# Optimization experiments

Measured on AMD Instinct MI355X. Metric: run time of the kernel, lower is better.

## Reference

```python
import jax, jax.numpy as jnp
import numpy as np

SPATIAL_DECAY = 50.0
POS_SCALE = 1000.0  # spread positions so decay=50 gives realistic locality


def setup_inputs() -> dict:
    key = jax.random.key(0)
    k1, k2 = jax.random.split(key)
    N, D = 8192, 512
    features = jax.random.normal(k1, (N, D), dtype=jnp.float32)
    positions = jax.random.uniform(k2, (N, 2), dtype=jnp.float32) * POS_SCALE
    lambda_weight = jnp.asarray(0.5, dtype=jnp.float32)  # nn.Parameter init
    temperature = jnp.asarray(1.0, dtype=jnp.float32)    # nn.Parameter init
    return {"features": features, "positions": positions,
            "lambda_weight": lambda_weight, "temperature": temperature, "k": 20}


def reference(features, positions, lambda_weight, temperature, k):
    N = features.shape[0]
    # F.normalize(dim=1), eps=1e-12
    norms = jnp.linalg.norm(features, axis=1, keepdims=True)
    feat_norm = features / jnp.maximum(norms, 1e-12)
    sim = feat_norm @ feat_norm.T                                   # (N, N)
    # squared euclidean distances (cdist(p=2) then **2 == squared dist)
    sq = jnp.sum(positions * positions, axis=1)                      # (N,)
    d2 = jnp.maximum(sq[:, None] + sq[None, :] - 2.0 * (positions @ positions.T), 0.0)
    spatial = jnp.exp(-d2 / (2.0 * SPATIAL_DECAY ** 2))             # (N, N)
    lam = jax.nn.sigmoid(lambda_weight)
    adj = jax.nn.sigmoid((lam * sim + (1.0 - lam) * spatial) * temperature)
    # row-wise top-k mask, scatter 1.0 at top-k columns
    _, topk_idx = jax.lax.top_k(adj, k)                              # (N, k)
    rows = jnp.arange(N)[:, None]
    mask = jnp.zeros_like(adj).at[rows, topk_idx].set(1.0)
    return adj * mask, lam
```

## Files before the change

### kernel.cpp

```cpp
#include <hip/hip_runtime.h>
#include <hip/hip_fp16.h>
#include <math.h>

#define N 8192
#define D 512
#define KSEL 20
#define CAND_CAP 384
#define WINDOW 2.5e-3f
#define BS_EXTRA 6.2e-4f
#define ROWU 8192

typedef __attribute__((ext_vector_type(8))) short short8;
typedef __attribute__((ext_vector_type(4))) float f32x4;

__device__ __forceinline__ unsigned short f2bf(float x) {
  unsigned int u = __float_as_uint(x);
  unsigned int r = u + 0x7FFFu + ((u >> 16) & 1u);
  return (unsigned short)(r >> 16);
}

__device__ __forceinline__ unsigned int packh2(float a, float b) {
  return (unsigned int)__half_as_ushort(__float2half(a)) |
         ((unsigned int)__half_as_ushort(__float2half(b)) << 16);
}

__device__ __forceinline__ void gld16(const unsigned short* g, unsigned short* l) {
  __builtin_amdgcn_global_load_lds(
      (const __attribute__((address_space(1))) unsigned int*)g,
      (__attribute__((address_space(3))) unsigned int*)l, 16, 0, 0);
}

__global__ __launch_bounds__(256) void prep_kernel(
    const float* __restrict__ feat, const float* __restrict__ pos,
    const float* __restrict__ lamw,
    float* __restrict__ normf, float* __restrict__ sqf,
    float* __restrict__ out) {
  int row = blockIdx.x * 256 + threadIdx.x;
  if (row >= N) return;
  const float* f = feat + (size_t)row * D;
  float part[4];
  #pragma unroll
  for (int b = 0; b < 4; b++) {
    const float* a = f + b * 128;
    float r[8];
    #pragma unroll
    for (int j = 0; j < 8; j++) r[j] = __fmul_rn(a[j], a[j]);
    for (int i = 8; i < 128; i += 8) {
      #pragma unroll
      for (int j = 0; j < 8; j++)
        r[j] = __fadd_rn(r[j], __fmul_rn(a[i + j], a[i + j]));
    }
    part[b] = __fadd_rn(__fadd_rn(__fadd_rn(r[0], r[1]), __fadd_rn(r[2], r[3])),
                        __fadd_rn(__fadd_rn(r[4], r[5]), __fadd_rn(r[6], r[7])));
  }
  float s = __fadd_rn(__fadd_rn(part[0], part[1]), __fadd_rn(part[2], part[3]));
  float nrm = fmaxf(__fsqrt_rn(s), 1e-12f);
  normf[row] = nrm;
  float x = pos[2 * row], y = pos[2 * row + 1];
  sqf[row] = __fadd_rn(__fmul_rn(x, x), __fmul_rn(y, y));
  if (row == 0) {
    float e = (float)exp(-(double)lamw[0]);
    out[(size_t)N * N] = 1.0f / __fadd_rn(1.0f, e);
  }
}

__global__ __launch_bounds__(256) void fnorm_kernel(
    const float* __restrict__ feat, const float* __restrict__ normf,
    float* __restrict__ fn32, unsigned short* __restrict__ fnbf) {
  int i0 = (blockIdx.x * 256 + threadIdx.x) * 4;
  float n = normf[i0 >> 9];
  float4 v = *(const float4*)(feat + i0);
  float4 q;
  q.x = v.x / n; q.y = v.y / n; q.z = v.z / n; q.w = v.w / n;
  *(float4*)(fn32 + i0) = q;
  uint2 o;
  o.x = (unsigned int)f2bf(q.x) | ((unsigned int)f2bf(q.y) << 16);
  o.y = (unsigned int)f2bf(q.z) | ((unsigned int)f2bf(q.w) << 16);
  *(uint2*)(fnbf + i0) = o;
}

__global__ __launch_bounds__(256) void adj_kernel(
    const unsigned short* __restrict__ G,
    const float* __restrict__ pos, const float* __restrict__ sqf,
    const float* __restrict__ lamw, const float* __restrict__ temp,
    unsigned int* out_u) {
  __shared__ __align__(16) unsigned char smem[32768];
  unsigned short* As = (unsigned short*)smem;
  unsigned short* Bs = As + 8192;
  unsigned int* tileT = (unsigned int*)smem;

  int L = blockIdx.x;
  int tid = threadIdx.x;

  if (L < 2048) {
    uint4 z = {0u, 0u, 0u, 0u};
    #pragma unroll
    for (int it = 0; it < 16; it++) {
      int g = L * 16384 + it * 1024 + tid * 4;
      int r = g >> 12, c = g & 4095;
      *(uint4*)(out_u + (size_t)r * ROWU + 4096 + c) = z;
    }
  }

  int by = (int)((129.0 - sqrt(129.0 * 129.0 - 8.0 * (double)L)) * 0.5);
  while (64 * (by + 1) - ((by + 1) * by) / 2 <= L) by++;
  while (64 * by - (by * (by - 1)) / 2 > L) by--;
  int bx = by + (L - (64 * by - (by * (by - 1)) / 2));

  int wave = tid >> 6, lane = tid & 63;
  int wr = (wave >> 1) * 64, wc = (wave & 1) * 64;
  int m = lane & 15, quad = lane >> 4;

  f32x4 acc[4][4];
  #pragma unroll
  for (int i = 0; i < 4; i++)
    #pragma unroll
    for (int j = 0; j < 4; j++) acc[i][j] = (f32x4){0.f, 0.f, 0.f, 0.f};

  for (int kt = 0; kt < D / 64; kt++) {
    #pragma unroll
    for (int i = 0; i < 4; i++) {
      int f = i * 256 + tid;
      int r = f >> 3, c = f & 7;
      int cs = (c + r) & 7;
      size_t goff = (size_t)r * D + kt * 64 + cs * 8;
      gld16(G + (size_t)(by * 128) * D + goff, &As[f * 8]);
      gld16(G + (size_t)(bx * 128) * D + goff, &Bs[f * 8]);
    }
    __syncthreads();
    #pragma unroll
    for (int h = 0; h < 2; h++) {
      short8 fa[4], fb[4];
      #pragma unroll
      for (int ti = 0; ti < 4; ti++) {
        int row = wr + ti * 16 + m;
        int cc = ((h * 4 + quad) - row) & 7;
        fa[ti] = *(const short8*)&As[row * 64 + cc * 8];
      }
      #pragma unroll
      for (int tj = 0; tj < 4; tj++) {
        int row = wc + tj * 16 + m;
        int cc = ((h * 4 + quad) - row) & 7;
        fb[tj] = *(const short8*)&Bs[row * 64 + cc * 8];
      }
      #pragma unroll
      for (int ti = 0; ti < 4; ti++)
        #pragma unroll
        for (int tj = 0; tj < 4; tj++)
          acc[ti][tj] = __builtin_amdgcn_mfma_f32_16x16x32_bf16(
              fa[ti], fb[tj], acc[ti][tj], 0, 0, 0);
    }
    __syncthreads();
  }

  float lam = 1.f / (1.f + __expf(-lamw[0]));
  float T = temp[0];
  float oml = 1.f - lam;
  bool offdiag = (bx != by);
  #pragma unroll
  for (int ti = 0; ti < 4; ti++) {
    int gi0 = by * 128 + wr + ti * 16 + quad * 4;
    float xi[4], yi[4], sqi[4];
    #pragma unroll
    for (int r = 0; r < 4; r++) {
      int gi = gi0 + r;
      xi[r] = pos[2 * gi]; yi[r] = pos[2 * gi + 1]; sqi[r] = sqf[gi];
    }
    #pragma unroll
    for (int tj = 0; tj < 4; tj++) {
      int gj = bx * 128 + wc + tj * 16 + m;
      float xj = pos[2 * gj], yj = pos[2 * gj + 1], sj = sqf[gj];
      f32x4 c = acc[ti][tj];
      float sv[4];
      #pragma unroll
      for (int r = 0; r < 4; r++) {
        float d2 = fmaxf(sqi[r] + sj - 2.f * (xi[r] * xj + yi[r] * yj), 0.f);
        float sp = __expf(-d2 * (1.f / 5000.f));
        sv[r] = (lam * c[r] + oml * sp) * T;
      }
      #pragma unroll
      for (int r = 0; r < 4; r++) {
        float pv = __shfl_xor(sv[r], 1, 64);
        if (!(lane & 1))
          out_u[(size_t)(gi0 + r) * ROWU + (gj >> 1)] = packh2(sv[r], pv);
      }
      if (offdiag) {
        int colL = wc + tj * 16 + m;
        int p0 = (wr + ti * 16) / 2 + quad * 2;
        tileT[colL * 64 + (p0 ^ (colL & 31))]       = packh2(sv[0], sv[1]);
        tileT[colL * 64 + ((p0 + 1) ^ (colL & 31))] = packh2(sv[2], sv[3]);
      }
    }
  }
  if (offdiag) {
    __syncthreads();
    int p = tid & 63, c0 = tid >> 6;
    for (int it = 0; it < 32; it++) {
      int c = it * 4 + c0;
      unsigned int w = tileT[c * 64 + (p ^ (c & 31))];
      out_u[(size_t)(bx * 128 + c) * ROWU + (by * 64 + p)] = w;
    }
  }
}

__global__ __launch_bounds__(256, 6) void topk_kernel(
    const float* __restrict__ pos, const float* __restrict__ sqf,
    const float* __restrict__ lamw, const float* __restrict__ temp,
    const float* __restrict__ fn32, float* __restrict__ out) {
  __shared__ float Tm[64 * 64];
  __shared__ float ai[D];
  __shared__ int   redi[2][4];
  __shared__ int   candIdx[CAND_CAP];
  __shared__ float candV[CAND_CAP];
  __shared__ int   selIdx[KSEL];
  __shared__ float selVal[KSEL];
  __shared__ int   cnt;

  int row = blockIdx.x, t = threadIdx.x;
  int lane = t & 63, wid = t >> 6;
  float* orow = out + (size_t)row * N;
  const uint4* ou4 = (const uint4*)orow;
  const float* fn_i = fn32 + (size_t)row * D;

  float rv[32];
  #pragma unroll
  for (int q = 0; q < 4; q++) {
    uint4 u = ou4[t + 256 * q];
    unsigned int w[4] = {u.x, u.y, u.z, u.w};
    #pragma unroll
    for (int d = 0; d < 4; d++) {
      __half2 h2 = *reinterpret_cast<__half2*>(&w[d]);
      rv[8 * q + 2 * d]     = __low2float(h2);
      rv[8 * q + 2 * d + 1] = __high2float(h2);
    }
  }
  for (int k = t; k < D; k += 256) ai[k] = fn_i[k];
  if (t == 0) cnt = 0;
  __syncthreads();

  {
    float4 z4 = {0.f, 0.f, 0.f, 0.f};
    #pragma unroll
    for (int i = 0; i < 4; i++) *(float4*)&orow[4 * t + 1024 * i] = z4;
  }

  float lo = -1.0f, hi = 1.5f;
  for (int it = 0; it < 12; it++) {
    float mid = 0.5f * (lo + hi);
    int c = 0;
    #pragma unroll
    for (int q = 0; q < 32; q++) c += (rv[q] >= mid) ? 1 : 0;
    #pragma unroll
    for (int off = 32; off > 0; off >>= 1) c += __shfl_down(c, off, 64);
    if (lane == 0) redi[it & 1][wid] = c;
    __syncthreads();
    int tot = redi[it & 1][0] + redi[it & 1][1] + redi[it & 1][2] + redi[it & 1][3];
    if (tot >= KSEL) lo = mid; else hi = mid;
  }

  float thr = lo - (WINDOW + BS_EXTRA);
  #pragma unroll
  for (int q = 0; q < 32; q++) {
    if (rv[q] >= thr) {
      int p = atomicAdd(&cnt, 1);
      if (p < CAND_CAP) candIdx[p] = 8 * (t + 256 * (q >> 3)) + (q & 7);
    }
  }
  __syncthreads();
  int ncand = min(cnt, CAND_CAP);

  float lamf;
  { float e = (float)exp(-(double)lamw[0]); lamf = 1.0f / __fadd_rn(1.0f, e); }
  float omlf = __fadd_rn(1.0f, -lamf);
  float Tf = temp[0];
  float sq_i = sqf[row];
  float xi = pos[2 * row], yi = pos[2 * row + 1];
  int c4 = t >> 2, sub = t & 3;
  int slot = (c4 + 16 * sub) & 63;

  for (int g = 0; g < ncand; g += 64) {
    int sidx = g + c4;
    int sj = candIdx[(sidx < ncand) ? sidx : 0];
    const float* fj = fn32 + (size_t)sj * D + sub * 16;
    float accv = 0.0f;
    int myIdx = g + t;
    float4 pv[4];
    #pragma unroll
    for (int q = 0; q < 4; q++) pv[q] = *(const float4*)(fj + 0 * 64 + q * 4);
    for (int ck = 0; ck < 8; ck++) {
      __syncthreads();
      #pragma unroll
      for (int q = 0; q < 4; q++) {
        int kl = sub * 16 + q * 4;
        Tm[(kl + 0) * 64 + slot] = pv[q].x;
        Tm[(kl + 1) * 64 + slot] = pv[q].y;
        Tm[(kl + 2) * 64 + slot] = pv[q].z;
        Tm[(kl + 3) * 64 + slot] = pv[q].w;
      }
      __syncthreads();
      if (ck < 7) {
        #pragma unroll
        for (int q = 0; q < 4; q++) pv[q] = *(const float4*)(fj + (ck + 1) * 64 + q * 4);
      }
      if (t < 64) {
        int kk = ck * 64;
        for (int kl = 0; kl < 64; kl++) {
          int s = (t + 16 * (kl >> 4)) & 63;
          accv = __fmaf_rn(ai[kk + kl], Tm[kl * 64 + s], accv);
        }
      }
    }
    if (t < 64 && myIdx < ncand) {
      int j = candIdx[myIdx];
      float xj = pos[2 * j], yj = pos[2 * j + 1];
      float dot2 = __fmaf_rn(yi, yj, __fmul_rn(xi, xj));
      float Ssum = __fadd_rn(sq_i, sqf[j]);
      float d2 = fmaxf(__fadd_rn(Ssum, -__fmul_rn(2.0f, dot2)), 0.0f);
      float arg = (-d2) / 5000.0f;
      float sp = (float)exp((double)arg);
      float u = __fmul_rn(__fadd_rn(__fmul_rn(lamf, accv), __fmul_rn(omlf, sp)), Tf);
      float e = (float)exp(-(double)u);
      candV[myIdx] = 1.0f / __fadd_rn(1.0f, e);
    }
  }

  if (t < 64) {
    for (int s = 0; s < KSEL; s++) {
      float bu = -1.0f; int bj = N, bs = 0;
      for (int c = t; c < ncand; c += 64) {
        float v = candV[c]; int j = candIdx[c];
        if (v > bu || (v == bu && j < bj)) { bu = v; bj = j; bs = c; }
      }
      #pragma unroll
      for (int off = 32; off > 0; off >>= 1) {
        float ov = __shfl_down(bu, off, 64);
        int   oj = __shfl_down(bj, off, 64);
        int   os = __shfl_down(bs, off, 64);
        if (ov > bu || (ov == bu && oj < bj)) { bu = ov; bj = oj; bs = os; }
      }
      if (t == 0) { selIdx[s] = bj; selVal[s] = bu; candV[bs] = -1.0f; }
      __builtin_amdgcn_s_waitcnt(0);
    }
  }
  __syncthreads();
  if (t < KSEL) orow[selIdx[t]] = selVal[t];
}

extern "C" void kernel_launch(void* const* d_in, const int* in_sizes, int n_in,
                              void* d_out, int out_size, void* d_ws, size_t ws_size,
                              hipStream_t stream) {
  const float* feat = (const float*)d_in[0];
  const float* pos  = (const float*)d_in[1];
  const float* lamw = (const float*)d_in[2];
  const float* temp = (const float*)d_in[3];
  float* out = (float*)d_out;
  unsigned int* out_u = (unsigned int*)d_out;
  float* normf = (float*)d_ws;
  float* sqf   = normf + N;
  float* fn32  = sqf + N;
  unsigned short* fnbf = (unsigned short*)(fn32 + (size_t)N * D);

  prep_kernel<<<N / 256, 256, 0, stream>>>(feat, pos, lamw, normf, sqf, out);
  fnorm_kernel<<<(N * D) / 1024, 256, 0, stream>>>(feat, normf, fn32, fnbf);
  adj_kernel<<<2080, 256, 0, stream>>>(fnbf, pos, sqf, lamw, temp, out_u);
  topk_kernel<<<N, 256, 0, stream>>>(pos, sqf, lamw, temp, fn32, out);
}
```

Baseline: 588.1 us.

## Stage fp16 adjacency in workspace buffer, zero output in adj kernel, fuse prep

Merges the norm and normalize kernels into one warp-per-row prep kernel. When the workspace is large enough, the adjacency kernel writes the fp16 scores to a separate compact buffer through a swizzled LDS tile with 16-byte stores, and the transposed half is stored with vectorized writes too. The output is zeroed in contiguous chunks inside the adjacency kernel, so top-k no longer has to zero its row after reading it. The cost is extra workspace memory plus a fallback path that keeps the old in-place layout.

```diff
diff --git a/kernel.cpp b/kernel.cpp
--- a/kernel.cpp
+++ b/kernel.cpp
@@ -9,6 +9,7 @@
 #define WINDOW 2.5e-3f
 #define BS_EXTRA 6.2e-4f
 #define ROWU 8192
+#define FS_A 4096
 
 typedef __attribute__((ext_vector_type(8))) short short8;
 typedef __attribute__((ext_vector_type(4))) float f32x4;
@@ -30,60 +31,77 @@
       (__attribute__((address_space(3))) unsigned int*)l, 16, 0, 0);
 }
 
+__device__ __forceinline__ int swz(int row, int cp) {
+  return row * 64 + ((((cp >> 2) ^ (row & 15)) << 2) | (cp & 3));
+}
+__device__ __forceinline__ int swz4(int row, int q) {
+  return row * 64 + ((q ^ (row & 15)) << 2);
+}
+
 __global__ __launch_bounds__(256) void prep_kernel(
     const float* __restrict__ feat, const float* __restrict__ pos,
     const float* __restrict__ lamw,
     float* __restrict__ normf, float* __restrict__ sqf,
+    float* __restrict__ fn32, unsigned short* __restrict__ fnbf,
     float* __restrict__ out) {
-  int row = blockIdx.x * 256 + threadIdx.x;
-  if (row >= N) return;
-  const float* f = feat + (size_t)row * D;
-  float part[4];
-  #pragma unroll
-  for (int b = 0; b < 4; b++) {
-    const float* a = f + b * 128;
-    float r[8];
-    #pragma unroll
-    for (int j = 0; j < 8; j++) r[j] = __fmul_rn(a[j], a[j]);
-    for (int i = 8; i < 128; i += 8) {
-      #pragma unroll
-      for (int j = 0; j < 8; j++)
-        r[j] = __fadd_rn(r[j], __fmul_rn(a[i + j], a[i + j]));
-    }
-    part[b] = __fadd_rn(__fadd_rn(__fadd_rn(r[0], r[1]), __fadd_rn(r[2], r[3])),
-                        __fadd_rn(__fadd_rn(r[4], r[5]), __fadd_rn(r[6], r[7])));
-  }
-  float s = __fadd_rn(__fadd_rn(part[0], part[1]), __fadd_rn(part[2], part[3]));
-  float nrm = fmaxf(__fsqrt_rn(s), 1e-12f);
-  normf[row] = nrm;
-  float x = pos[2 * row], y = pos[2 * row + 1];
-  sqf[row] = __fadd_rn(__fmul_rn(x, x), __fmul_rn(y, y));
-  if (row == 0) {
-    float e = (float)exp(-(double)lamw[0]);
-    out[(size_t)N * N] = 1.0f / __fadd_rn(1.0f, e);
-  }
-}
-
-__global__ __launch_bounds__(256) void fnorm_kernel(
-    const float* __restrict__ feat, const float* __restrict__ normf,
-    float* __restrict__ fn32, unsigned short* __restrict__ fnbf) {
-  int i0 = (blockIdx.x * 256 + threadIdx.x) * 4;
-  float n = normf[i0 >> 9];
-  float4 v = *(const float4*)(feat + i0);
-  float4 q;
-  q.x = v.x / n; q.y = v.y / n; q.z = v.z / n; q.w = v.w / n;
-  *(float4*)(fn32 + i0) = q;
-  uint2 o;
-  o.x = (unsigned int)f2bf(q.x) | ((unsigned int)f2bf(q.y) << 16);
-  o.y = (unsigned int)f2bf(q.z) | ((unsigned int)f2bf(q.w) << 16);
-  *(uint2*)(fnbf + i0) = o;
+  __shared__ float rowbuf[4][512];
+  int w = threadIdx.x >> 6, lane = threadIdx.x & 63;
+  float* rb = rowbuf[w];
+  for (int i = 0; i < 8; i++) {
+    int row = blockIdx.x * 32 + w * 8 + i;
+    const float* f = feat + (size_t)row * D;
+    float4 v0 = *(const float4*)(f + 4 * lane);
+    float4 v1 = *(const float4*)(f + 256 + 4 * lane);
+    *(float4*)&rb[4 * lane] = v0;
+    *(float4*)&rb[256 + 4 * lane] = v1;
+    __builtin_amdgcn_s_waitcnt(0);
+    float s = 0.f;
+    if (lane < 32) {
+      int b = lane >> 3, j = lane & 7;
+      const float* a = rb + b * 128 + j;
+      float r = __fmul_rn(a[0], a[0]);
+      #pragma unroll
+      for (int k = 1; k < 16; k++)
+        r = __fadd_rn(r, __fmul_rn(a[8 * k], a[8 * k]));
+      r = __fadd_rn(r, __shfl_xor(r, 1, 64));
+      r = __fadd_rn(r, __shfl_xor(r, 2, 64));
+      r = __fadd_rn(r, __shfl_xor(r, 4, 64));
+      r = __fadd_rn(r, __shfl_xor(r, 8, 64));
+      r = __fadd_rn(r, __shfl_xor(r, 16, 64));
+      s = r;
+    }
+    float st = __shfl(s, 0, 64);
+    float nrm = fmaxf(__fsqrt_rn(st), 1e-12f);
+    if (lane == 0) {
+      normf[row] = nrm;
+      float x = pos[2 * row], y = pos[2 * row + 1];
+      sqf[row] = __fadd_rn(__fmul_rn(x, x), __fmul_rn(y, y));
+      if (row == 0) {
+        float e = (float)exp(-(double)lamw[0]);
+        out[(size_t)N * N] = 1.0f / __fadd_rn(1.0f, e);
+      }
+    }
+    float4 q0, q1;
+    q0.x = v0.x / nrm; q0.y = v0.y / nrm; q0.z = v0.z / nrm; q0.w = v0.w / nrm;
+    q1.x = v1.x / nrm; q1.y = v1.y / nrm; q1.z = v1.z / nrm; q1.w = v1.w / nrm;
+    *(float4*)(fn32 + (size_t)row * D + 4 * lane) = q0;
+    *(float4*)(fn32 + (size_t)row * D + 256 + 4 * lane) = q1;
+    uint2 o0, o1;
+    o0.x = (unsigned int)f2bf(q0.x) | ((unsigned int)f2bf(q0.y) << 16);
+    o0.y = (unsigned int)f2bf(q0.z) | ((unsigned int)f2bf(q0.w) << 16);
+    o1.x = (unsigned int)f2bf(q1.x) | ((unsigned int)f2bf(q1.y) << 16);
+    o1.y = (unsigned int)f2bf(q1.z) | ((unsigned int)f2bf(q1.w) << 16);
+    *(uint2*)(fnbf + (size_t)row * D + 4 * lane) = o0;
+    *(uint2*)(fnbf + (size_t)row * D + 256 + 4 * lane) = o1;
+  }
 }
 
 __global__ __launch_bounds__(256) void adj_kernel(
     const unsigned short* __restrict__ G,
     const float* __restrict__ pos, const float* __restrict__ sqf,
     const float* __restrict__ lamw, const float* __restrict__ temp,
-    unsigned int* out_u) {
+    unsigned int* __restrict__ filt, int fs,
+    unsigned int* __restrict__ out_u, int mode) {
   __shared__ __align__(16) unsigned char smem[32768];
   unsigned short* As = (unsigned short*)smem;
   unsigned short* Bs = As + 8192;
@@ -94,11 +112,18 @@
 
   if (L < 2048) {
     uint4 z = {0u, 0u, 0u, 0u};
-    #pragma unroll
-    for (int it = 0; it < 16; it++) {
-      int g = L * 16384 + it * 1024 + tid * 4;
-      int r = g >> 12, c = g & 4095;
-      *(uint4*)(out_u + (size_t)r * ROWU + 4096 + c) = z;
+    if (mode == 0) {
+      size_t base = (size_t)L * 32768;
+      #pragma unroll
+      for (int it = 0; it < 32; it++)
+        *(uint4*)(out_u + base + it * 1024 + tid * 4) = z;
+    } else {
+      #pragma unroll
+      for (int it = 0; it < 16; it++) {
+        int g = L * 16384 + it * 1024 + tid * 4;
+        int r = g >> 12, c = g & 4095;
+        *(uint4*)(out_u + (size_t)r * ROWU + 4096 + c) = z;
+      }
     }
   }
 
@@ -157,6 +182,7 @@
   float T = temp[0];
   float oml = 1.f - lam;
   bool offdiag = (bx != by);
+
   #pragma unroll
   for (int ti = 0; ti < 4; ti++) {
     int gi0 = by * 128 + wr + ti * 16 + quad * 4;
@@ -178,27 +204,44 @@
         float sp = __expf(-d2 * (1.f / 5000.f));
         sv[r] = (lam * c[r] + oml * sp) * T;
       }
+      int cpL = (wc + tj * 16 + m) >> 1;
       #pragma unroll
       for (int r = 0; r < 4; r++) {
         float pv = __shfl_xor(sv[r], 1, 64);
-        if (!(lane & 1))
-          out_u[(size_t)(gi0 + r) * ROWU + (gj >> 1)] = packh2(sv[r], pv);
-      }
-      if (offdiag) {
-        int colL = wc + tj * 16 + m;
-        int p0 = (wr + ti * 16) / 2 + quad * 2;
-        tileT[colL * 64 + (p0 ^ (colL & 31))]       = packh2(sv[0], sv[1]);
-        tileT[colL * 64 + ((p0 + 1) ^ (colL & 31))] = packh2(sv[2], sv[3]);
-      }
-    }
-  }
+        if (!(lane & 1)) {
+          int rowL = wr + ti * 16 + quad * 4 + r;
+          tileT[swz(rowL, cpL)] = packh2(sv[r], pv);
+        }
+      }
+    }
+  }
+  __syncthreads();
+
+  #pragma unroll
+  for (int it = 0; it < 8; it++) {
+    int idx4 = it * 256 + tid;
+    int row = idx4 >> 4, q = idx4 & 15;
+    uint4 v = *(uint4*)&tileT[swz4(row, q)];
+    *(uint4*)(filt + (size_t)(by * 128 + row) * fs + bx * 64 + q * 4) = v;
+  }
+
   if (offdiag) {
-    __syncthreads();
-    int p = tid & 63, c0 = tid >> 6;
-    for (int it = 0; it < 32; it++) {
-      int c = it * 4 + c0;
-      unsigned int w = tileT[c * 64 + (p ^ (c & 31))];
-      out_u[(size_t)(bx * 128 + c) * ROWU + (by * 64 + p)] = w;
+    #pragma unroll
+    for (int it = 0; it < 8; it++) {
+      int idx4 = it * 256 + tid;
+      int c = idx4 >> 4, q = idx4 & 15;
+      unsigned int wv[4];
+      #pragma unroll
+      for (int d = 0; d < 4; d++) {
+        int p = q * 4 + d;
+        unsigned int lo = tileT[swz(2 * p, c >> 1)];
+        unsigned int hi = tileT[swz(2 * p + 1, c >> 1)];
+        unsigned int h0 = (c & 1) ? (lo >> 16) : (lo & 0xFFFFu);
+        unsigned int h1 = (c & 1) ? (hi >> 16) : (hi & 0xFFFFu);
+        wv[d] = h0 | (h1 << 16);
+      }
+      uint4 v; v.x = wv[0]; v.y = wv[1]; v.z = wv[2]; v.w = wv[3];
+      *(uint4*)(filt + (size_t)(bx * 128 + c) * fs + by * 64 + q * 4) = v;
     }
   }
 }
@@ -206,7 +249,9 @@
 __global__ __launch_bounds__(256, 6) void topk_kernel(
     const float* __restrict__ pos, const float* __restrict__ sqf,
     const float* __restrict__ lamw, const float* __restrict__ temp,
-    const float* __restrict__ fn32, float* __restrict__ out) {
+    const float* __restrict__ fn32,
+    const unsigned int* __restrict__ filt, int fs,
+    float* __restrict__ out, int doZero) {
   __shared__ float Tm[64 * 64];
   __shared__ float ai[D];
   __shared__ int   redi[2][4];
@@ -219,13 +264,13 @@
   int row = blockIdx.x, t = threadIdx.x;
   int lane = t & 63, wid = t >> 6;
   float* orow = out + (size_t)row * N;
-  const uint4* ou4 = (const uint4*)orow;
+  const uint4* fu4 = (const uint4*)(filt + (size_t)row * fs);
   const float* fn_i = fn32 + (size_t)row * D;
 
   float rv[32];
   #pragma unroll
   for (int q = 0; q < 4; q++) {
-    uint4 u = ou4[t + 256 * q];
+    uint4 u = fu4[t + 256 * q];
     unsigned int w[4] = {u.x, u.y, u.z, u.w};
     #pragma unroll
     for (int d = 0; d < 4; d++) {
@@ -238,7 +283,7 @@
   if (t == 0) cnt = 0;
   __syncthreads();
 
-  {
+  if (doZero) {
     float4 z4 = {0.f, 0.f, 0.f, 0.f};
     #pragma unroll
     for (int i = 0; i < 4; i++) *(float4*)&orow[4 * t + 1024 * i] = z4;
@@ -286,7 +331,7 @@
     int myIdx = g + t;
     float4 pv[4];
     #pragma unroll
-    for (int q = 0; q < 4; q++) pv[q] = *(const float4*)(fj + 0 * 64 + q * 4);
+    for (int q = 0; q < 4; q++) pv[q] = *(const float4*)(fj + q * 4);
     for (int ck = 0; ck < 8; ck++) {
       __syncthreads();
       #pragma unroll
@@ -355,13 +400,28 @@
   const float* temp = (const float*)d_in[3];
   float* out = (float*)d_out;
   unsigned int* out_u = (unsigned int*)d_out;
+
   float* normf = (float*)d_ws;
   float* sqf   = normf + N;
   float* fn32  = sqf + N;
   unsigned short* fnbf = (unsigned short*)(fn32 + (size_t)N * D);
-
-  prep_kernel<<<N / 256, 256, 0, stream>>>(feat, pos, lamw, normf, sqf, out);
-  fnorm_kernel<<<(N * D) / 1024, 256, 0, stream>>>(feat, normf, fn32, fnbf);
-  adj_kernel<<<2080, 256, 0, stream>>>(fnbf, pos, sqf, lamw, temp, out_u);
-  topk_kernel<<<N, 256, 0, stream>>>(pos, sqf, lamw, temp, fn32, out);
-}
+  unsigned int* filtA = (unsigned int*)(fnbf + (size_t)N * D);
+  size_t needA = (size_t)2 * N * 4 + (size_t)N * D * 4 + (size_t)N * D * 2 +
+                 (size_t)N * FS_A * 4;
+  size_t needB = (size_t)2 * N * 4 + (size_t)N * D * 4 + (size_t)N * D * 2;
+
+  prep_kernel<<<N / 32, 256, 0, stream>>>(feat, pos, lamw, normf, sqf,
+                                          fn32, fnbf, out);
+  if (ws_size >= needA) {
+    adj_kernel<<<2080, 256, 0, stream>>>(fnbf, pos, sqf, lamw, temp,
+                                         filtA, FS_A, out_u, 0);
+    topk_kernel<<<N, 256, 0, stream>>>(pos, sqf, lamw, temp, fn32,
+                                       filtA, FS_A, out, 0);
+  } else {
+    (void)needB;
+    adj_kernel<<<2080, 256, 0, stream>>>(fnbf, pos, sqf, lamw, temp,
+                                         out_u, ROWU, out_u, 1);
+    topk_kernel<<<N, 256, 0, stream>>>(pos, sqf, lamw, temp, fn32,
+                                       out_u, ROWU, out, 1);
+  }
+}
```

Measured after the change: 582.0 us. Within noise of the previous version (-1.0%).
